# Performance work log

Hardware: AMD Instinct MI355X
Metric: run time of the kernel (lower is better)

## Reference

```python
import jax, jax.numpy as jnp
import numpy as np

N = 131072
IN_DIM = 12
HID = 256
NUM_LAYERS = 10
OUT_DIM = 3


def _xavier(key, fan_in, fan_out, gain):
    bound = gain * jnp.sqrt(6.0 / (fan_in + fan_out))
    return jax.random.uniform(key, (fan_in, fan_out), jnp.float32, -bound, bound)


def setup_inputs() -> dict:
    key = jax.random.key(0)
    ks = jax.random.split(key, 12)
    x = jax.random.normal(ks[0], (N, IN_DIM), jnp.float32)
    W0 = _xavier(ks[1], IN_DIM, HID, 5.0)
    b0 = jnp.zeros((HID,), jnp.float32)
    Ws = jnp.stack([_xavier(ks[2 + i], HID, HID, 5.0) for i in range(NUM_LAYERS - 1)])
    bs = jnp.zeros((NUM_LAYERS - 1, HID), jnp.float32)
    Wout = _xavier(ks[11], HID, OUT_DIM, 1.0)
    bout = jnp.zeros((OUT_DIM,), jnp.float32)
    return {"x": x, "W0": W0, "b0": b0, "Ws": Ws, "bs": bs, "Wout": Wout, "bout": bout}


def _act(h, i):
    m = i % 4
    if m == 0:
        return jnp.sin(h)
    if m == 1:
        return jnp.cos(h)
    if m == 2:
        return jnp.exp(-h * h)  # gaussian
    return jnp.tanh(h)


def reference(x, W0, b0, Ws, bs, Wout, bout):
    h = _act(x @ W0 + b0, 0)
    for i in range(1, NUM_LAYERS):  # small fixed layer loop
        h = _act(h @ Ws[i - 1] + bs[i - 1], i)
    return jax.nn.sigmoid(h @ Wout + bout)  # (N, 3) in [0, 1]
```

## Files before the change

kernel.cpp:

```cpp
#include <hip/hip_runtime.h>
#include <type_traits>

#define HID 256
#define PTS 64
typedef unsigned short ushort_t;
typedef unsigned int uint_t;
typedef __attribute__((ext_vector_type(8))) _Float16 half8v;
typedef __attribute__((ext_vector_type(2))) __fp16 pk16x2;
typedef __attribute__((ext_vector_type(4))) float f32x4;
typedef __attribute__((ext_vector_type(16))) float f32x16;

#define LO_SCALE   4096.0f
#define LO_INV     0.000244140625f

template <int M>
__device__ __forceinline__ float act(float z) {
    if constexpr (M == 0) return __sinf(z);
    else if constexpr (M == 1) return __cosf(z);
    else if constexpr (M == 2) return __expf(-z * z);
    else { float e = __expf(2.0f * z); return 1.0f - 2.0f / (e + 1.0f); }
}

__device__ __forceinline__ float trunc16(float v) {
    return __builtin_bit_cast(float, __builtin_bit_cast(uint_t, v) & 0xFFFFE000u);
}
__device__ __forceinline__ uint_t pkrtz(float a, float b) {
    pk16x2 r = __builtin_amdgcn_cvt_pkrtz(a, b);
    return __builtin_bit_cast(uint_t, r);
}

#define NFRAG (9 * 16 * 8)
#define PREP_THREADS (NFRAG * 64)

__global__ void prep_w(const float* __restrict__ Ws,
                       _Float16* __restrict__ WHI, _Float16* __restrict__ WLO) {
    int t = blockIdx.x * 256 + threadIdx.x;
    if (t >= PREP_THREADS) return;
    int l  = t & 63;
    int f  = t >> 6;
    int jt = f & 7;
    int ks = (f >> 3) & 15;
    int L  = f >> 7;
    int j  = jt * 32 + (l & 31);
    int kb = ks * 16 + (l >> 5) * 8;
    const float* Wp = Ws + (size_t)L * 65536;
    _Float16* oh = WHI + (size_t)t * 8;
    _Float16* ol = WLO + (size_t)t * 8;
    #pragma unroll
    for (int e = 0; e < 8; ++e) {
        float wv = Wp[(size_t)(kb + e) * 256 + j];
        float hi32 = trunc16(wv);
        oh[e] = (_Float16)hi32;
        ol[e] = (_Float16)((wv - hi32) * LO_SCALE);
    }
}

__global__ __launch_bounds__(512, 4) void cppn_mfma(
    const float* __restrict__ x,
    const float* __restrict__ W0,
    const float* __restrict__ b0,
    const float* __restrict__ bs,
    const float* __restrict__ Wout,
    const float* __restrict__ bout,
    const _Float16* __restrict__ WHI,
    const _Float16* __restrict__ WLO,
    float* __restrict__ out,
    int n)
{
    __shared__ ushort_t ha[64 * 256];
    __shared__ ushort_t hb[64 * 256];

    const int tid = threadIdx.x;
    const int l   = tid & 63;
    const int w   = tid >> 6;
    const long p0 = (long)blockIdx.x * PTS;

    {
        const int p  = l;
        const long pg = p0 + p;
        float xv[12];
        if (pg < n) {
            const float4* xr = (const float4*)(x + pg * 12);
            float4 a = xr[0], b = xr[1], c = xr[2];
            xv[0]=a.x; xv[1]=a.y; xv[2]=a.z;  xv[3]=a.w;
            xv[4]=b.x; xv[5]=b.y; xv[6]=b.z;  xv[7]=b.w;
            xv[8]=c.x; xv[9]=c.y; xv[10]=c.z; xv[11]=c.w;
        } else {
            #pragma unroll
            for (int k = 0; k < 12; ++k) xv[k] = 0.0f;
        }
        const int jb = w * 32;
        float z[32];
        #pragma unroll
        for (int jj = 0; jj < 32; ++jj) z[jj] = b0[jb + jj];
        #pragma unroll
        for (int k = 0; k < 12; ++k) {
            const float a = xv[k];
            #pragma unroll
            for (int jj = 0; jj < 32; ++jj)
                z[jj] = fmaf(a, W0[k * HID + jb + jj], z[jj]);
        }
        const int swz = (p & 7) << 3;
        #pragma unroll
        for (int jj = 0; jj < 32; jj += 2) {
            float v0 = act<0>(z[jj]), v1 = act<0>(z[jj + 1]);
            float t0 = trunc16(v0), t1 = trunc16(v1);
            uint_t ph = pkrtz(t0, t1);
            uint_t pl = pkrtz((v0 - t0) * LO_SCALE, (v1 - t1) * LO_SCALE);
            int ei = p * 256 + ((jb + jj) ^ swz);
            *(uint_t*)&ha[ei] = ph;
            *(uint_t*)&hb[ei] = pl;
        }
    }
    __syncthreads();

    const int lm5  = l & 31;
    const int hi5  = l >> 5;
    const int aswz = (l & 7) << 3;
    const int rowb[2] = { (0 * 32 + lm5) * 256, (1 * 32 + lm5) * 256 };

    for (int Li = 0; Li < 9; ++Li) {
        const _Float16* __restrict__ WH = WHI + ((size_t)(Li * 128 + w) * 64 + (size_t)l) * 8;
        const _Float16* __restrict__ WL = WLO + ((size_t)(Li * 128 + w) * 64 + (size_t)l) * 8;

        f32x16 acc[2], accL[2];
        #pragma unroll
        for (int pt = 0; pt < 2; ++pt) {
            #pragma unroll
            for (int r = 0; r < 16; ++r) { acc[pt][r] = 0.f; accL[pt][r] = 0.f; }
        }

        half8v ah = *(const half8v*)(WH);
        half8v al = *(const half8v*)(WL);

        #pragma unroll 1
        for (int ks = 0; ks < 16; ++ks) {
            const int ksn = (ks + 1) & 15;
            half8v ahn = *(const half8v*)(WH + (size_t)ksn * 4096);
            half8v aln = *(const half8v*)(WL + (size_t)ksn * 4096);

            const int ke = (ks * 16 + hi5 * 8) ^ aswz;
            half8v bh0 = *(const half8v*)&ha[rowb[0] + ke];
            half8v bl0 = *(const half8v*)&hb[rowb[0] + ke];
            half8v bh1 = *(const half8v*)&ha[rowb[1] + ke];
            half8v bl1 = *(const half8v*)&hb[rowb[1] + ke];

            acc[0]  = __builtin_amdgcn_mfma_f32_32x32x16_f16(ah, bh0, acc[0],  0, 0, 0);
            acc[1]  = __builtin_amdgcn_mfma_f32_32x32x16_f16(ah, bh1, acc[1],  0, 0, 0);
            accL[0] = __builtin_amdgcn_mfma_f32_32x32x16_f16(ah, bl0, accL[0], 0, 0, 0);
            accL[1] = __builtin_amdgcn_mfma_f32_32x32x16_f16(ah, bl1, accL[1], 0, 0, 0);
            accL[0] = __builtin_amdgcn_mfma_f32_32x32x16_f16(al, bh0, accL[0], 0, 0, 0);
            accL[1] = __builtin_amdgcn_mfma_f32_32x32x16_f16(al, bh1, accL[1], 0, 0, 0);

            ah = ahn; al = aln;
        }
        __syncthreads();

        const float* bsL = bs + Li * 256;
        const int m = (Li + 1) & 3;
        auto storeact = [&](auto mt) {
            constexpr int M = decltype(mt)::value;
            #pragma unroll
            for (int d = 0; d < 4; ++d) {
                const int jrun = w * 32 + d * 8 + hi5 * 4;
                float4 b4 = *(const float4*)(bsL + jrun);
                #pragma unroll
                for (int pt = 0; pt < 2; ++pt) {
                    float v[4], th[4];
                    #pragma unroll
                    for (int c = 0; c < 4; ++c) {
                        const int r = d * 4 + c;
                        float bj = (c == 0) ? b4.x : (c == 1) ? b4.y : (c == 2) ? b4.z : b4.w;
                        float zv = acc[pt][r] + accL[pt][r] * LO_INV + bj;
                        v[c]  = act<M>(zv);
                        th[c] = trunc16(v[c]);
                    }
                    uint2 uh = make_uint2(pkrtz(th[0], th[1]), pkrtz(th[2], th[3]));
                    uint2 ul = make_uint2(pkrtz((v[0]-th[0])*LO_SCALE, (v[1]-th[1])*LO_SCALE),
                                          pkrtz((v[2]-th[2])*LO_SCALE, (v[3]-th[3])*LO_SCALE));
                    const int p  = pt * 32 + lm5;
                    const int ei = p * 256 + (jrun ^ aswz);
                    *(uint2*)&ha[ei] = uh;
                    *(uint2*)&hb[ei] = ul;
                }
            }
        };
        if      (m == 0) storeact(std::integral_constant<int,0>{});
        else if (m == 1) storeact(std::integral_constant<int,1>{});
        else if (m == 2) storeact(std::integral_constant<int,2>{});
        else             storeact(std::integral_constant<int,3>{});
        __syncthreads();
    }

    if (tid < 192) {
        const int p = tid & 63;
        const int c = tid >> 6;
        const long pg = p0 + p;
        if (pg < n) {
            const int swz = (p & 7) << 3;
            float zacc = bout[c];
            #pragma unroll 4
            for (int c2 = 0; c2 < 32; ++c2) {
                const int ei = p * 256 + ((c2 * 8) ^ swz);
                half8v vh = *(const half8v*)&ha[ei];
                half8v vl = *(const half8v*)&hb[ei];
                #pragma unroll
                for (int e = 0; e < 8; ++e) {
                    const int k = c2 * 8 + e;
                    float hv = (float)vh[e] + (float)vl[e] * LO_INV;
                    zacc = fmaf(hv, Wout[k * 3 + c], zacc);
                }
            }
            out[pg * 3 + c] = 1.0f / (1.0f + __expf(-zacc));
        }
    }
}

__global__ __launch_bounds__(512, 4) void cppn_fused_fp32(
    const float* __restrict__ x, const float* __restrict__ W0,
    const float* __restrict__ b0, const float* __restrict__ Ws,
    const float* __restrict__ bs, const float* __restrict__ Wout,
    const float* __restrict__ bout, float* __restrict__ out, int n)
{
    __shared__ float h[HID][PTS];
    const int tid  = threadIdx.x;
    const int p    = tid & 63;
    const int j0   = __builtin_amdgcn_readfirstlane((tid >> 6) << 5);
    const long pg  = (long)blockIdx.x * PTS + p;
    const bool live = (pg < n);
    {
        float xv[12];
        if (live) {
            const float4* xr = (const float4*)(x + pg * 12);
            float4 a = xr[0], b = xr[1], c = xr[2];
            xv[0]=a.x; xv[1]=a.y; xv[2]=a.z;  xv[3]=a.w;
            xv[4]=b.x; xv[5]=b.y; xv[6]=b.z;  xv[7]=b.w;
            xv[8]=c.x; xv[9]=c.y; xv[10]=c.z; xv[11]=c.w;
        } else {
            #pragma unroll
            for (int k = 0; k < 12; ++k) xv[k] = 0.0f;
        }
        float acc[32];
        #pragma unroll
        for (int q = 0; q < 32; ++q) acc[q] = 0.0f;
        #pragma unroll
        for (int k = 0; k < 12; ++k) {
            const float a = xv[k];
            const float4* wr = (const float4*)(W0 + k * HID + j0);
            #pragma unroll
            for (int q = 0; q < 8; ++q) {
                float4 wv = wr[q];
                acc[4*q+0] = fmaf(a, wv.x, acc[4*q+0]);
                acc[4*q+1] = fmaf(a, wv.y, acc[4*q+1]);
                acc[4*q+2] = fmaf(a, wv.z, acc[4*q+2]);
                acc[4*q+3] = fmaf(a, wv.w, acc[4*q+3]);
            }
        }
        #pragma unroll
        for (int q = 0; q < 8; ++q) {
            float4 b4 = *(const float4*)(b0 + j0 + 4*q);
            h[j0+4*q+0][p] = act<0>(acc[4*q+0] + b4.x);
            h[j0+4*q+1][p] = act<0>(acc[4*q+1] + b4.y);
            h[j0+4*q+2][p] = act<0>(acc[4*q+2] + b4.z);
            h[j0+4*q+3][p] = act<0>(acc[4*q+3] + b4.w);
        }
        __syncthreads();
    }
    auto layerF = [&](const float* __restrict__ W, const float* __restrict__ b, auto mtag) {
        constexpr int M = decltype(mtag)::value;
        float acc[32];
        #pragma unroll
        for (int q = 0; q < 32; ++q) acc[q] = 0.0f;
        #pragma unroll 2
        for (int k = 0; k < HID; ++k) {
            const float a = h[k][p];
            const float4* wr = (const float4*)(W + k * HID + j0);
            #pragma unroll
            for (int q = 0; q < 8; ++q) {
                float4 wv = wr[q];
                acc[4*q+0] = fmaf(a, wv.x, acc[4*q+0]);
                acc[4*q+1] = fmaf(a, wv.y, acc[4*q+1]);
                acc[4*q+2] = fmaf(a, wv.z, acc[4*q+2]);
                acc[4*q+3] = fmaf(a, wv.w, acc[4*q+3]);
            }
        }
        __syncthreads();
        #pragma unroll
        for (int q = 0; q < 8; ++q) {
            float4 b4 = *(const float4*)(b + j0 + 4*q);
            h[j0+4*q+0][p] = act<M>(acc[4*q+0] + b4.x);
            h[j0+4*q+1][p] = act<M>(acc[4*q+1] + b4.y);
            h[j0+4*q+2][p] = act<M>(acc[4*q+2] + b4.z);
            h[j0+4*q+3][p] = act<M>(acc[4*q+3] + b4.w);
        }
        __syncthreads();
    };
    layerF(Ws + 0*65536, bs + 0*256, std::integral_constant<int,1>{});
    layerF(Ws + 1*65536, bs + 1*256, std::integral_constant<int,2>{});
    layerF(Ws + 2*65536, bs + 2*256, std::integral_constant<int,3>{});
    layerF(Ws + 3*65536, bs + 3*256, std::integral_constant<int,0>{});
    layerF(Ws + 4*65536, bs + 4*256, std::integral_constant<int,1>{});
    layerF(Ws + 5*65536, bs + 5*256, std::integral_constant<int,2>{});
    layerF(Ws + 6*65536, bs + 6*256, std::integral_constant<int,3>{});
    layerF(Ws + 7*65536, bs + 7*256, std::integral_constant<int,0>{});
    layerF(Ws + 8*65536, bs + 8*256, std::integral_constant<int,1>{});
    if (tid < 192) {
        const int pp = tid & 63;
        const int c  = tid >> 6;
        const long pgo = (long)blockIdx.x * PTS + pp;
        if (pgo < n) {
            float z = bout[c];
            #pragma unroll 4
            for (int k = 0; k < HID; ++k)
                z = fmaf(h[k][pp], Wout[k * 3 + c], z);
            out[pgo * 3 + c] = 1.0f / (1.0f + __expf(-z));
        }
    }
}

extern "C" void kernel_launch(void* const* d_in, const int* in_sizes, int n_in,
                              void* d_out, int out_size, void* d_ws, size_t ws_size,
                              hipStream_t stream) {
    const float* x    = (const float*)d_in[0];
    const float* W0   = (const float*)d_in[1];
    const float* b0   = (const float*)d_in[2];
    const float* Ws   = (const float*)d_in[3];
    const float* bs   = (const float*)d_in[4];
    const float* Wout = (const float*)d_in[5];
    const float* bout = (const float*)d_in[6];
    float* out = (float*)d_out;

    const int n = in_sizes[0] / 12;
    const int grid = (n + PTS - 1) / PTS;

    const size_t whi_bytes = (size_t)PREP_THREADS * 8 * sizeof(_Float16);
    const size_t need = 2 * whi_bytes;

    if (ws_size >= need) {
        _Float16* WHI = (_Float16*)d_ws;
        _Float16* WLO = (_Float16*)((char*)d_ws + whi_bytes);
        prep_w<<<(PREP_THREADS + 255) / 256, 256, 0, stream>>>(Ws, WHI, WLO);
        cppn_mfma<<<grid, 512, 0, stream>>>(x, W0, b0, bs, Wout, bout, WHI, WLO, out, n);
    } else {
        cppn_fused_fp32<<<grid, 512, 0, stream>>>(x, W0, b0, Ws, bs, Wout, bout, out, n);
    }
}
```

Baseline: 515.8 us.

## Retile warp MFMA work: each warp covers two output-column blocks for half the points

Each of 8 warps previously computed 32 output columns for all 64 points, loading one weight fragment pair and four activation fragments per k-step. Now each warp handles 64 output columns for 32 points, loading two weight fragment pairs from global memory and only two activation fragments from LDS per step. This trades LDS read traffic for more global/L2 weight loads per warp and higher register use for prefetched weights.

Measured after the change: 562.9 us. 1.09x slower.

```diff
diff --git a/kernel.cpp b/kernel.cpp
--- a/kernel.cpp
+++ b/kernel.cpp
@@ -114,45 +114,54 @@
     }
     __syncthreads();
 
-    const int lm5  = l & 31;
-    const int hi5  = l >> 5;
-    const int aswz = (l & 7) << 3;
-    const int rowb[2] = { (0 * 32 + lm5) * 256, (1 * 32 + lm5) * 256 };
+    const int lm5   = l & 31;
+    const int hi5   = l >> 5;
+    const int jgrp  = w & 3;
+    const int phalf = w >> 2;
+    const int aswz  = (lm5 & 7) << 3;
+    const int rowb  = (phalf * 32 + lm5) * 256;
 
     for (int Li = 0; Li < 9; ++Li) {
-        const _Float16* __restrict__ WH = WHI + ((size_t)(Li * 128 + w) * 64 + (size_t)l) * 8;
-        const _Float16* __restrict__ WL = WLO + ((size_t)(Li * 128 + w) * 64 + (size_t)l) * 8;
+        const _Float16* __restrict__ WH =
+            WHI + ((size_t)((Li * 16) * 8 + jgrp * 2) * 64 + (size_t)l) * 8;
+        const _Float16* __restrict__ WL =
+            WLO + ((size_t)((Li * 16) * 8 + jgrp * 2) * 64 + (size_t)l) * 8;
 
         f32x16 acc[2], accL[2];
         #pragma unroll
-        for (int pt = 0; pt < 2; ++pt) {
-            #pragma unroll
-            for (int r = 0; r < 16; ++r) { acc[pt][r] = 0.f; accL[pt][r] = 0.f; }
-        }
-
-        half8v ah = *(const half8v*)(WH);
-        half8v al = *(const half8v*)(WL);
+        for (int jj = 0; jj < 2; ++jj) {
+            #pragma unroll
+            for (int r = 0; r < 16; ++r) { acc[jj][r] = 0.f; accL[jj][r] = 0.f; }
+        }
+
+        half8v ah[2], al[2];
+        ah[0] = *(const half8v*)(WH);
+        ah[1] = *(const half8v*)(WH + 512);
+        al[0] = *(const half8v*)(WL);
+        al[1] = *(const half8v*)(WL + 512);
 
         #pragma unroll 1
         for (int ks = 0; ks < 16; ++ks) {
             const int ksn = (ks + 1) & 15;
-            half8v ahn = *(const half8v*)(WH + (size_t)ksn * 4096);
-            half8v aln = *(const half8v*)(WL + (size_t)ksn * 4096);
+            half8v ahn[2], aln[2];
+            ahn[0] = *(const half8v*)(WH + (size_t)ksn * 4096);
+            ahn[1] = *(const half8v*)(WH + (size_t)ksn * 4096 + 512);
+            aln[0] = *(const half8v*)(WL + (size_t)ksn * 4096);
+            aln[1] = *(const half8v*)(WL + (size_t)ksn * 4096 + 512);
 
             const int ke = (ks * 16 + hi5 * 8) ^ aswz;
-            half8v bh0 = *(const half8v*)&ha[rowb[0] + ke];
-            half8v bl0 = *(const half8v*)&hb[rowb[0] + ke];
-            half8v bh1 = *(const half8v*)&ha[rowb[1] + ke];
-            half8v bl1 = *(const half8v*)&hb[rowb[1] + ke];
-
-            acc[0]  = __builtin_amdgcn_mfma_f32_32x32x16_f16(ah, bh0, acc[0],  0, 0, 0);
-            acc[1]  = __builtin_amdgcn_mfma_f32_32x32x16_f16(ah, bh1, acc[1],  0, 0, 0);
-            accL[0] = __builtin_amdgcn_mfma_f32_32x32x16_f16(ah, bl0, accL[0], 0, 0, 0);
-            accL[1] = __builtin_amdgcn_mfma_f32_32x32x16_f16(ah, bl1, accL[1], 0, 0, 0);
-            accL[0] = __builtin_amdgcn_mfma_f32_32x32x16_f16(al, bh0, accL[0], 0, 0, 0);
-            accL[1] = __builtin_amdgcn_mfma_f32_32x32x16_f16(al, bh1, accL[1], 0, 0, 0);
-
-            ah = ahn; al = aln;
+            half8v bh = *(const half8v*)&ha[rowb + ke];
+            half8v bl = *(const half8v*)&hb[rowb + ke];
+
+            acc[0]  = __builtin_amdgcn_mfma_f32_32x32x16_f16(ah[0], bh, acc[0],  0, 0, 0);
+            acc[1]  = __builtin_amdgcn_mfma_f32_32x32x16_f16(ah[1], bh, acc[1],  0, 0, 0);
+            accL[0] = __builtin_amdgcn_mfma_f32_32x32x16_f16(ah[0], bl, accL[0], 0, 0, 0);
+            accL[1] = __builtin_amdgcn_mfma_f32_32x32x16_f16(ah[1], bl, accL[1], 0, 0, 0);
+            accL[0] = __builtin_amdgcn_mfma_f32_32x32x16_f16(al[0], bh, accL[0], 0, 0, 0);
+            accL[1] = __builtin_amdgcn_mfma_f32_32x32x16_f16(al[1], bh, accL[1], 0, 0, 0);
+
+            ah[0] = ahn[0]; ah[1] = ahn[1];
+            al[0] = aln[0]; al[1] = aln[1];
         }
         __syncthreads();
 
@@ -160,25 +169,25 @@
         const int m = (Li + 1) & 3;
         auto storeact = [&](auto mt) {
             constexpr int M = decltype(mt)::value;
-            #pragma unroll
-            for (int d = 0; d < 4; ++d) {
-                const int jrun = w * 32 + d * 8 + hi5 * 4;
-                float4 b4 = *(const float4*)(bsL + jrun);
+            const int p  = phalf * 32 + lm5;
+            #pragma unroll
+            for (int jj = 0; jj < 2; ++jj) {
                 #pragma unroll
-                for (int pt = 0; pt < 2; ++pt) {
+                for (int d = 0; d < 4; ++d) {
+                    const int jrun = jgrp * 64 + jj * 32 + d * 8 + hi5 * 4;
+                    float4 b4 = *(const float4*)(bsL + jrun);
                     float v[4], th[4];
                     #pragma unroll
                     for (int c = 0; c < 4; ++c) {
                         const int r = d * 4 + c;
                         float bj = (c == 0) ? b4.x : (c == 1) ? b4.y : (c == 2) ? b4.z : b4.w;
-                        float zv = acc[pt][r] + accL[pt][r] * LO_INV + bj;
+                        float zv = acc[jj][r] + accL[jj][r] * LO_INV + bj;
                         v[c]  = act<M>(zv);
                         th[c] = trunc16(v[c]);
                     }
                     uint2 uh = make_uint2(pkrtz(th[0], th[1]), pkrtz(th[2], th[3]));
                     uint2 ul = make_uint2(pkrtz((v[0]-th[0])*LO_SCALE, (v[1]-th[1])*LO_SCALE),
                                           pkrtz((v[2]-th[2])*LO_SCALE, (v[3]-th[3])*LO_SCALE));
-                    const int p  = pt * 32 + lm5;
                     const int ei = p * 256 + (jrun ^ aswz);
                     *(uint2*)&ha[ei] = uh;
                     *(uint2*)&hb[ei] = ul;
```
